# Kernel tuning notes

Measured on AMD Instinct MI355X. Metric: run time of the kernel, lower is better.

The kernel has to match this reference:

```python
import jax, jax.numpy as jnp
import numpy as np

N = 100000      # total nodes (10 graphs x 10000)
E = 1600000     # edges, avg degree 16
HN = 64         # hidden_node_dim
HE = 16         # hidden_edge_dim
IN_N, IN_E = 3, 1
L = 3           # conv_layers
B = 10          # num_graphs
NEG_SLOPE = 0.2
BN_EPS = 1e-5


def setup_inputs() -> dict:
    key = jax.random.key(0)
    ks = jax.random.split(key, 8)
    s = lambda d: 1.0 / np.sqrt(d)
    return {
        "x": jax.random.normal(ks[0], (N, IN_N), jnp.float32),
        "edge_attr": jax.random.uniform(ks[1], (E, IN_E), jnp.float32),
        "edge_index": jax.random.randint(ks[2], (2, E), 0, N, jnp.int64),
        "fc_node_w": jax.random.normal(ks[3], (IN_N, HN), jnp.float32) * s(IN_N),
        "fc_node_b": jnp.zeros((HN,), jnp.float32),
        "fc_edge_w": jax.random.normal(ks[4], (IN_E, HE), jnp.float32) * s(IN_E),
        "fc_edge_b": jnp.zeros((HE,), jnp.float32),
        "bn_gamma": jnp.ones((HN,), jnp.float32),
        "bn_beta": jnp.zeros((HN,), jnp.float32),
        "fc_w": jax.random.normal(ks[5], (L, HN, HN), jnp.float32) * s(HN),
        "fc_b": jnp.zeros((L, HN), jnp.float32),
        "attn_w": jax.random.normal(ks[6], (L, 2 * HN + HE, HN), jnp.float32) * s(2 * HN + HE),
        "attn_b": jnp.zeros((L, HN), jnp.float32),
        "batch_size": B,
    }


def segment_softmax(alpha, idx, num_segments):
    # PyG softmax: per-target-node, per-channel, numerically stable
    amax = jax.ops.segment_max(alpha, idx, num_segments=num_segments)
    amax = jnp.where(jnp.isfinite(amax), amax, 0.0)  # empty segments -> -inf
    ex = jnp.exp(alpha - amax[idx])
    denom = jax.ops.segment_sum(ex, idx, num_segments=num_segments)
    return ex / (denom[idx] + 1e-16)


def reference(x, edge_attr, edge_index, fc_node_w, fc_node_b, fc_edge_w, fc_edge_b,
              bn_gamma, bn_beta, fc_w, fc_b, attn_w, attn_b, batch_size):
    h = x @ fc_node_w + fc_node_b                 # [N, HN]
    e = edge_attr @ fc_edge_w + fc_edge_b        # [E, HE]
    # BatchNorm1d (training-mode batch statistics, biased variance)
    mean = jnp.mean(h, axis=0)
    var = jnp.mean((h - mean) ** 2, axis=0)
    h = (h - mean) * jax.lax.rsqrt(var + BN_EPS) * bn_gamma + bn_beta

    src, dst = edge_index[0], edge_index[1]      # x_j = h[src], x_i = h[dst]
    for l in range(L):
        hl = h @ fc_w[l] + fc_b[l]               # [N, HN]
        xi = hl[dst]                             # [E, HN]
        xj = hl[src]                             # [E, HN]
        cat = jnp.concatenate([xi, xj, e], axis=-1)  # [E, 2*HN+HE]
        alpha = cat @ attn_w[l] + attn_b[l]      # [E, HN]
        alpha = jax.nn.leaky_relu(alpha, NEG_SLOPE)
        alpha = segment_softmax(alpha, dst, N)
        h = jax.ops.segment_sum(xj * alpha, dst, num_segments=N)  # scatter-add aggregate
    return h.reshape(batch_size, -1, HN)
```

## Files before the change

kernel.cpp:

```cpp
#include <hip/hip_runtime.h>
#include <math.h>

#define NN 100000
#define NE 1600000
#define LAYERS 3
#define NEG 0.2f
#define BN_EPS 1e-5f
#define LOG2E 1.4426950408889634f

#define NB 196
#define NWG 512
#define CHUNK 3125
#define MOMB 304
#define TFB 1563

typedef __attribute__((ext_vector_type(8))) short bf16x8;
typedef __attribute__((ext_vector_type(4))) float f32x4;

#if __has_builtin(__builtin_amdgcn_exp2f)
#define EXP2(x) __builtin_amdgcn_exp2f(x)
#else
#define EXP2(x) __expf((x) * 0.6931471805599453f)
#endif

__device__ __forceinline__ unsigned f2bf(float x) {
    unsigned u = __float_as_uint(x);
    return (u + 0x7fffu + ((u >> 16) & 1u)) >> 16;
}

__global__ __launch_bounds__(256) void k_front(const int* __restrict__ ei,
    int* __restrict__ counts, const float* __restrict__ x, float* __restrict__ mom)
{
    int t = threadIdx.x;
    if (blockIdx.x < NWG) {
        __shared__ int hist[NB];
        int wg = blockIdx.x;
        if (t < NB) hist[t] = 0;
        __syncthreads();
        int base = wg * CHUNK;
        for (int i = t; i < CHUNK; i += 256)
            atomicAdd(&hist[ei[NE + base + i] >> 9], 1);
        __syncthreads();
        if (t < NB) counts[wg * NB + t] = hist[t];
    } else {
        int mb = blockIdx.x - NWG;
        float s0=0,s1=0,s2=0,m00=0,m01=0,m02=0,m11=0,m12=0,m22=0;
        for (int n = mb * 256 + t; n < NN; n += MOMB * 256) {
            float a = x[n*3], b = x[n*3+1], c = x[n*3+2];
            s0 += a; s1 += b; s2 += c;
            m00 = fmaf(a,a,m00); m01 = fmaf(a,b,m01); m02 = fmaf(a,c,m02);
            m11 = fmaf(b,b,m11); m12 = fmaf(b,c,m12); m22 = fmaf(c,c,m22);
        }
        #pragma unroll
        for (int off = 32; off; off >>= 1) {
            s0 += __shfl_xor(s0, off); s1 += __shfl_xor(s1, off); s2 += __shfl_xor(s2, off);
            m00 += __shfl_xor(m00, off); m01 += __shfl_xor(m01, off); m02 += __shfl_xor(m02, off);
            m11 += __shfl_xor(m11, off); m12 += __shfl_xor(m12, off); m22 += __shfl_xor(m22, off);
        }
        __shared__ float red[4][9];
        int wave = t >> 6, lane = t & 63;
        if (lane == 0) {
            red[wave][0]=s0; red[wave][1]=s1; red[wave][2]=s2;
            red[wave][3]=m00; red[wave][4]=m01; red[wave][5]=m02;
            red[wave][6]=m11; red[wave][7]=m12; red[wave][8]=m22;
        }
        __syncthreads();
        if (t < 9) {
            float v = red[0][t] + red[1][t] + red[2][t] + red[3][t];
            atomicAdd(&mom[t], v);
        }
    }
}

__device__ __forceinline__ float bn_scale_of(const float* __restrict__ mom,
    const float* __restrict__ fnw, const float* __restrict__ fnb,
    const float* __restrict__ gamma, int k)
{
    float w0 = fnw[k], w1 = fnw[64 + k], w2 = fnw[128 + k], bc = fnb[k];
    float dot  = mom[0]*w0 + mom[1]*w1 + mom[2]*w2;
    float quad = mom[3]*w0*w0 + 2.f*mom[4]*w0*w1 + 2.f*mom[5]*w0*w2
               + mom[6]*w1*w1 + 2.f*mom[7]*w1*w2 + mom[8]*w2*w2;
    float mean = dot * (1.0f / NN) + bc;
    float eh2  = quad * (1.0f / NN) + 2.f * bc * dot * (1.0f / NN) + bc * bc;
    float var  = eh2 - mean * mean;
    return gamma[k] * rsqrtf(var + BN_EPS);
}

__global__ __launch_bounds__(256) void k_mid(const float* __restrict__ mom,
    const float* __restrict__ fnw, const float* __restrict__ fnb,
    const float* __restrict__ gamma, const float* __restrict__ beta,
    const float* __restrict__ few, const float* __restrict__ feb,
    const float* __restrict__ attn_w, const float* __restrict__ attn_b,
    const float* __restrict__ fcb, const float* __restrict__ fcw,
    int* __restrict__ counts, int* __restrict__ bbase, int* __restrict__ row_ptr,
    float* __restrict__ u, float* __restrict__ c0, float* __restrict__ feff,
    unsigned short* __restrict__ wt)
{
    int t = threadIdx.x;
    if (blockIdx.x == 0) {
        __shared__ float ssh[64], sfe[3][64];
        if (t < 64) {
            float w0 = fnw[t], w1 = fnw[64 + t], w2 = fnw[128 + t], bc = fnb[t];
            float dot  = mom[0]*w0 + mom[1]*w1 + mom[2]*w2;
            float quad = mom[3]*w0*w0 + 2.f*mom[4]*w0*w1 + 2.f*mom[5]*w0*w2
                       + mom[6]*w1*w1 + 2.f*mom[7]*w1*w2 + mom[8]*w2*w2;
            float mean = dot * (1.0f / NN) + bc;
            float eh2  = quad * (1.0f / NN) + 2.f * bc * dot * (1.0f / NN) + bc * bc;
            float var  = eh2 - mean * mean;
            float sc   = gamma[t] * rsqrtf(var + BN_EPS);
            ssh[t] = beta[t] - mean * sc;
        }
        __syncthreads();
        if (t < 64) {
            float v = 0.f;
            for (int k = 0; k < 64; k++) v = fmaf(ssh[k], fcw[k * 64 + t], v);
            sfe[0][t] = fcb[t] + v;
            sfe[1][t] = fcb[64 + t];
            sfe[2][t] = fcb[128 + t];
        }
        __syncthreads();
        if (t < 192) {
            int l = t >> 6, c = t & 63;
            const float* AW = attn_w + l * 144 * 64;
            float uu = 0.f, cc = 0.f;
            for (int j = 0; j < 16; j++) {
                float wv = AW[(128 + j) * 64 + c];
                uu = fmaf(few[j], wv, uu);
                cc = fmaf(feb[j], wv, cc);
            }
            float bi = 0.f;
            for (int tt = 0; tt < 64; tt++)
                bi = fmaf(sfe[l][tt], AW[tt * 64 + c] + AW[(64 + tt) * 64 + c], bi);
            u[t]    = uu * LOG2E;
            c0[t]   = (cc + attn_b[t] + bi) * LOG2E;
            feff[t] = sfe[l][c];
        }
    } else if (blockIdx.x == 1) {
        __shared__ int s_tot[256];
        int tot = 0;
        if (t < NB)
            for (int w = 0; w < NWG; w++) tot += counts[w * NB + t];
        s_tot[t] = tot;
        __syncthreads();
        for (int off = 1; off < 256; off <<= 1) {
            int v = (t >= off) ? s_tot[t - off] : 0;
            __syncthreads();
            s_tot[t] += v;
            __syncthreads();
        }
        int excl = s_tot[t] - tot;
        if (t < NB) {
            bbase[t] = excl;
            int run = excl;
            for (int w = 0; w < NWG; w++) {
                int c = counts[w * NB + t];
                counts[w * NB + t] = run;
                run += c;
            }
            if (t == NB - 1) {
                bbase[NB] = run;
                row_ptr[NN] = run;
            }
        }
    } else {
        int task = (blockIdx.x - 2) * 4 + (t >> 6);
        int k = t & 63;
        int l = task / 192, g = task - l * 192;
        const float* W0 = fcw + l * 4096;
        float scale = (l == 0) ? bn_scale_of(mom, fnw, fnb, gamma, k) : 1.0f;
        float v;
        if (g < 64) {
            v = W0[k * 64 + g] * scale;
        } else {
            int c = g & 63;
            const float* Wx = attn_w + l * 144 * 64 + (g < 128 ? 0 : 4096);
            float s = 0.f;
            for (int tt = 0; tt < 64; tt++) s = fmaf(W0[k * 64 + tt], Wx[tt * 64 + c], s);
            v = s * scale * LOG2E;
        }
        wt[(l * 192 + g) * 64 + k] = (unsigned short)f2bf(v);
    }
}

__device__ __forceinline__ void tf_core(const bf16x8* a, const unsigned short* __restrict__ wt_l,
    const float* __restrict__ feff_l, const float* __restrict__ c0_l,
    float* __restrict__ ai, unsigned* __restrict__ packed, int n0, int r16, int quad)
{
    f32x4 acc[12];
    #pragma unroll
    for (int i = 0; i < 12; i++) acc[i] = (f32x4){0.f, 0.f, 0.f, 0.f};
    const unsigned short* wb = wt_l + (size_t)r16 * 64 + quad * 8;
    #pragma unroll
    for (int cb = 0; cb < 12; cb++) {
        bf16x8 b0 = *(const bf16x8*)(wb + cb * 1024);
        bf16x8 b1 = *(const bf16x8*)(wb + cb * 1024 + 32);
        acc[cb] = __builtin_amdgcn_mfma_f32_16x16x32_bf16(a[0], b0, acc[cb], 0, 0, 0);
        acc[cb] = __builtin_amdgcn_mfma_f32_16x16x32_bf16(a[1], b1, acc[cb], 0, 0, 0);
    }
    #pragma unroll
    for (int r = 0; r < 4; r++) {
        int nd = n0 + quad * 4 + r;
        if (nd < NN) {
            size_t base = (size_t)nd * 64 + r16;
            #pragma unroll
            for (int cq = 0; cq < 4; cq++) {
                float hlv = acc[cq][r] + feff_l[cq * 16 + r16];
                float aiv = acc[4 + cq][r] + c0_l[cq * 16 + r16];
                float ajv = acc[8 + cq][r];
                ai[base + cq * 16]     = aiv;
                packed[base + cq * 16] = f2bf(hlv) | (f2bf(ajv) << 16);
            }
        }
    }
}

__global__ __launch_bounds__(256) void k_l3(const int* __restrict__ ei,
    const float* __restrict__ ea, const int* __restrict__ counts, int2* __restrict__ brec,
    const float* __restrict__ xin, const float* __restrict__ fnw, const float* __restrict__ fnb,
    const unsigned short* __restrict__ wt, const float* __restrict__ feff,
    const float* __restrict__ c0v, float* __restrict__ ai, unsigned* __restrict__ packed)
{
    int t = threadIdx.x;
    if (blockIdx.x < NWG) {
        __shared__ int off[NB];
        int wg = blockIdx.x;
        if (t < NB) off[t] = counts[wg * NB + t];
        __syncthreads();
        int base = wg * CHUNK;
        for (int i = t; i < CHUNK; i += 256) {
            int k = base + i;
            int s = ei[k], d = ei[NE + k];
            int b = d >> 9;
            int j = atomicAdd(&off[b], 1);
            brec[j] = make_int2(((d & 511) << 17) | s, __float_as_int(ea[k]));
        }
    } else {
        int bid = blockIdx.x - NWG;
        int wv = t >> 6, l = t & 63;
        int r16 = l & 15, quad = l >> 4;
        int n0 = bid * 64 + wv * 16;
        int na = n0 + r16; if (na >= NN) na = NN - 1;
        float x0 = xin[na*3], x1 = xin[na*3+1], x2 = xin[na*3+2];
        bf16x8 a[2];
        #pragma unroll
        for (int ks = 0; ks < 2; ks++) {
            bf16x8 tt;
            #pragma unroll
            for (int e = 0; e < 8; e++) {
                int c = quad * 8 + ks * 32 + e;
                float v = fmaf(x0, fnw[c], fmaf(x1, fnw[64 + c], fmaf(x2, fnw[128 + c], fnb[c])));
                tt[e] = (short)f2bf(v);
            }
            a[ks] = tt;
        }
        tf_core(a, wt, feff, c0v, ai, packed, n0, r16, quad);
    }
}

__global__ __launch_bounds__(256) void k_csr(const int2* __restrict__ brec,
    const int* __restrict__ bbase, int* __restrict__ row_ptr, int2* __restrict__ er)
{
    __shared__ int s_cnt[512], s_excl[512], s_ts[256];
    int t = threadIdx.x, b = blockIdx.x;
    int beg = bbase[b], end = bbase[b + 1];
    s_cnt[t] = 0; s_cnt[t + 256] = 0;
    __syncthreads();
    for (int i = beg + t; i < end; i += 256)
        atomicAdd(&s_cnt[brec[i].x >> 17], 1);
    __syncthreads();
    int a0 = s_cnt[2 * t], a1 = s_cnt[2 * t + 1];
    int ts = a0 + a1;
    s_ts[t] = ts;
    __syncthreads();
    for (int off = 1; off < 256; off <<= 1) {
        int v = (t >= off) ? s_ts[t - off] : 0;
        __syncthreads();
        s_ts[t] += v;
        __syncthreads();
    }
    int et = s_ts[t] - ts;
    s_excl[2 * t] = et; s_excl[2 * t + 1] = et + a0;
    s_cnt[t] = 0; s_cnt[t + 256] = 0;
    __syncthreads();
    #pragma unroll
    for (int q = 0; q < 2; q++) {
        int dl = t + q * 256;
        int n = b * 512 + dl;
        if (n < NN) row_ptr[n] = beg + s_excl[dl];
    }
    for (int i = beg + t; i < end; i += 256) {
        int2 r = brec[i];
        int dl = r.x >> 17;
        int pos = atomicAdd(&s_cnt[dl], 1);
        er[beg + s_excl[dl] + pos] = make_int2(r.x & 0x1FFFF, r.y);
    }
}

#define EDGE_STEP(q, dacc, sacc) { \
    float aa = fmaf(__int_as_float(e[q].y), uc, base + __uint_as_float(p[q] & 0xffff0000u)); \
    aa = fmaxf(aa, NEG * aa); \
    float xx = EXP2(aa); \
    dacc += xx; sacc = fmaf(xx, __uint_as_float(p[q] << 16), sacc); }

template<int DOTF>
__global__ __launch_bounds__(256) void k_edgetf(const unsigned* __restrict__ packed_r,
    float* __restrict__ ai, const int* __restrict__ row_ptr,
    const int2* __restrict__ er, const float* __restrict__ u_l,
    const unsigned short* __restrict__ wt_n, const float* __restrict__ feff_n,
    const float* __restrict__ c0_n, unsigned* __restrict__ packed_w,
    float* __restrict__ outp)
{
    __shared__ float hlds[64][68];
    int t = threadIdx.x;
    int wv = t >> 6, lane = t & 63;
    int nbase = blockIdx.x * 64 + wv * 16;
    float uc = u_l[lane];
    const unsigned* __restrict__ pc = packed_r + lane;
    for (int m = 0; m < 16; m++) {
        int n = nbase + m;
        if (n >= NN) break;
        int beg = row_ptr[n], end = row_ptr[n + 1];
        float base = ai[(size_t)n * 64 + lane];
        float d0 = 0.f, d1 = 0.f, s0 = 0.f, s1 = 0.f;
        int k = beg;
        for (; k + 16 <= end; k += 16) {
            int2 e[16]; unsigned p[16];
            #pragma unroll
            for (int q = 0; q < 16; q++) e[q] = er[k + q];
            #pragma unroll
            for (int q = 0; q < 16; q++) p[q] = pc[(size_t)e[q].x << 6];
            #pragma unroll
            for (int q = 0; q < 16; q++) {
                if (q & 1) EDGE_STEP(q, d1, s1) else EDGE_STEP(q, d0, s0)
            }
        }
        for (; k + 8 <= end; k += 8) {
            int2 e[8]; unsigned p[8];
            #pragma unroll
            for (int q = 0; q < 8; q++) e[q] = er[k + q];
            #pragma unroll
            for (int q = 0; q < 8; q++) p[q] = pc[(size_t)e[q].x << 6];
            #pragma unroll
            for (int q = 0; q < 8; q++) {
                if (q & 1) EDGE_STEP(q, d1, s1) else EDGE_STEP(q, d0, s0)
            }
        }
        for (; k + 4 <= end; k += 4) {
            int2 e[4]; unsigned p[4];
            #pragma unroll
            for (int q = 0; q < 4; q++) e[q] = er[k + q];
            #pragma unroll
            for (int q = 0; q < 4; q++) p[q] = pc[(size_t)e[q].x << 6];
            #pragma unroll
            for (int q = 0; q < 4; q++) {
                if (q & 1) EDGE_STEP(q, d1, s1) else EDGE_STEP(q, d0, s0)
            }
        }
        for (; k < end; k++) {
            int2 e[1]; unsigned p[1];
            e[0] = er[k];
            p[0] = pc[(size_t)e[0].x << 6];
            EDGE_STEP(0, d0, s0)
        }
        float hv = (s0 + s1) / (d0 + d1 + 1e-16f);
        if (DOTF) hlds[wv * 16 + m][lane] = hv;
        else      outp[(size_t)n * 64 + lane] = hv;
    }
    if (DOTF) {
        int r16 = lane & 15, quad = lane >> 4;
        const float* hp = &hlds[wv * 16 + r16][quad * 8];
        bf16x8 a[2];
        #pragma unroll
        for (int ks = 0; ks < 2; ks++) {
            f32x4 lo = *(const f32x4*)(hp + ks * 32);
            f32x4 hi = *(const f32x4*)(hp + ks * 32 + 4);
            bf16x8 tt;
            tt[0] = (short)f2bf(lo[0]); tt[1] = (short)f2bf(lo[1]);
            tt[2] = (short)f2bf(lo[2]); tt[3] = (short)f2bf(lo[3]);
            tt[4] = (short)f2bf(hi[0]); tt[5] = (short)f2bf(hi[1]);
            tt[6] = (short)f2bf(hi[2]); tt[7] = (short)f2bf(hi[3]);
            a[ks] = tt;
        }
        tf_core(a, wt_n, feff_n, c0_n, ai, packed_w, nbase, r16, quad);
    }
}

extern "C" void kernel_launch(void* const* d_in, const int* in_sizes, int n_in,
                              void* d_out, int out_size, void* d_ws, size_t ws_size,
                              hipStream_t stream)
{
    const float* x    = (const float*)d_in[0];
    const float* ea   = (const float*)d_in[1];
    const int*   ei   = (const int*)d_in[2];
    const float* fnw  = (const float*)d_in[3];
    const float* fnb  = (const float*)d_in[4];
    const float* few  = (const float*)d_in[5];
    const float* feb  = (const float*)d_in[6];
    const float* gmm  = (const float*)d_in[7];
    const float* beta = (const float*)d_in[8];
    const float* fcw  = (const float*)d_in[9];
    const float* fcb  = (const float*)d_in[10];
    const float* aw   = (const float*)d_in[11];
    const float* ab   = (const float*)d_in[12];
    float* out = (float*)d_out;

    char* ws = (char*)d_ws;
    size_t off = 0;
    auto alloc = [&](size_t bytes) -> void* {
        void* p = ws + off;
        off += (bytes + 255) / 256 * 256;
        return p;
    };
    float*    ai      = (float*)   alloc((size_t)NN * 64 * 4);
    unsigned* packed0 = (unsigned*)alloc((size_t)NN * 64 * 4);
    unsigned* packed1 = (unsigned*)alloc((size_t)NN * 64 * 4);
    int2*     er      = (int2*)    alloc((size_t)NE * 8);
    int2*     brec    = (int2*)    alloc((size_t)NE * 8);
    int*      row_ptr = (int*)     alloc((size_t)(NN + 1) * 4);
    int*      counts  = (int*)     alloc((size_t)NB * NWG * 4);
    int*      bbase   = (int*)     alloc((NB + 1) * 4);
    float*    mom     = (float*)   alloc(12 * 4);
    float*    uvec    = (float*)   alloc(192 * 4);
    float*    c0vec   = (float*)   alloc(192 * 4);
    float*    feff    = (float*)   alloc(192 * 4);
    unsigned short* wt = (unsigned short*)alloc((size_t)LAYERS * 192 * 64 * 2);

    (void)hipMemsetAsync(mom, 0, 12 * 4, stream);

    k_front<<<NWG + MOMB, 256, 0, stream>>>(ei, counts, x, mom);
    k_mid<<<2 + 144, 256, 0, stream>>>(mom, fnw, fnb, gmm, beta, few, feb, aw, ab,
                                       fcb, fcw, counts, bbase, row_ptr,
                                       uvec, c0vec, feff, wt);
    k_l3<<<NWG + TFB, 256, 0, stream>>>(ei, ea, counts, brec, x, fnw, fnb,
                                        wt, feff, c0vec, ai, packed0);
    k_csr<<<NB, 256, 0, stream>>>(brec, bbase, row_ptr, er);
    k_edgetf<1><<<TFB, 256, 0, stream>>>(packed0, ai, row_ptr, er, uvec,
                                         wt + (size_t)192 * 64, feff + 64, c0vec + 64,
                                         packed1, out);
    k_edgetf<1><<<TFB, 256, 0, stream>>>(packed1, ai, row_ptr, er, uvec + 64,
                                         wt + (size_t)2 * 192 * 64, feff + 128, c0vec + 128,
                                         packed0, out);
    k_edgetf<0><<<TFB, 256, 0, stream>>>(packed0, ai, row_ptr, er, uvec + 128,
                                         wt, feff, c0vec, packed1, out);
    (void)in_sizes; (void)n_in; (void)out_size; (void)ws_size;
}
```

Measured before the change: 497.1 us.

## Assign one node per wave in edge-aggregation kernel with 1024-thread blocks

The edge softmax-aggregation kernel now gives each wave a single destination node instead of looping over 16 nodes per wave. Blocks grow to 16 waves (1024 threads), and 16 times as many waves are in flight across the GPU. After a block barrier, four of the waves each compute one 16-column slice of the next layer's transform with MFMA. The transform helper is also reorganised to hold fewer accumulators at once, which lowers register pressure. The aim is to hide gather latency and balance uneven node degrees, at the cost of a block-wide sync and 12 idle waves during the MFMA step.

```diff
diff --git a/kernel.cpp b/kernel.cpp
--- a/kernel.cpp
+++ b/kernel.cpp
@@ -13,6 +13,7 @@
 #define CHUNK 3125
 #define MOMB 304
 #define TFB 1563
+#define ETB 6250
 
 typedef __attribute__((ext_vector_type(8))) short bf16x8;
 typedef __attribute__((ext_vector_type(4))) float f32x4;
@@ -186,29 +187,24 @@
     const float* __restrict__ feff_l, const float* __restrict__ c0_l,
     float* __restrict__ ai, unsigned* __restrict__ packed, int n0, int r16, int quad)
 {
-    f32x4 acc[12];
-    #pragma unroll
-    for (int i = 0; i < 12; i++) acc[i] = (f32x4){0.f, 0.f, 0.f, 0.f};
     const unsigned short* wb = wt_l + (size_t)r16 * 64 + quad * 8;
     #pragma unroll
-    for (int cb = 0; cb < 12; cb++) {
-        bf16x8 b0 = *(const bf16x8*)(wb + cb * 1024);
-        bf16x8 b1 = *(const bf16x8*)(wb + cb * 1024 + 32);
-        acc[cb] = __builtin_amdgcn_mfma_f32_16x16x32_bf16(a[0], b0, acc[cb], 0, 0, 0);
-        acc[cb] = __builtin_amdgcn_mfma_f32_16x16x32_bf16(a[1], b1, acc[cb], 0, 0, 0);
-    }
-    #pragma unroll
-    for (int r = 0; r < 4; r++) {
-        int nd = n0 + quad * 4 + r;
-        if (nd < NN) {
-            size_t base = (size_t)nd * 64 + r16;
-            #pragma unroll
-            for (int cq = 0; cq < 4; cq++) {
-                float hlv = acc[cq][r] + feff_l[cq * 16 + r16];
-                float aiv = acc[4 + cq][r] + c0_l[cq * 16 + r16];
-                float ajv = acc[8 + cq][r];
-                ai[base + cq * 16]     = aiv;
-                packed[base + cq * 16] = f2bf(hlv) | (f2bf(ajv) << 16);
+    for (int cq = 0; cq < 4; cq++) {
+        f32x4 ah = {0.f,0.f,0.f,0.f}, aa = {0.f,0.f,0.f,0.f}, aj = {0.f,0.f,0.f,0.f};
+        ah = __builtin_amdgcn_mfma_f32_16x16x32_bf16(a[0], *(const bf16x8*)(wb + cq * 1024), ah, 0, 0, 0);
+        ah = __builtin_amdgcn_mfma_f32_16x16x32_bf16(a[1], *(const bf16x8*)(wb + cq * 1024 + 32), ah, 0, 0, 0);
+        aa = __builtin_amdgcn_mfma_f32_16x16x32_bf16(a[0], *(const bf16x8*)(wb + (4 + cq) * 1024), aa, 0, 0, 0);
+        aa = __builtin_amdgcn_mfma_f32_16x16x32_bf16(a[1], *(const bf16x8*)(wb + (4 + cq) * 1024 + 32), aa, 0, 0, 0);
+        aj = __builtin_amdgcn_mfma_f32_16x16x32_bf16(a[0], *(const bf16x8*)(wb + (8 + cq) * 1024), aj, 0, 0, 0);
+        aj = __builtin_amdgcn_mfma_f32_16x16x32_bf16(a[1], *(const bf16x8*)(wb + (8 + cq) * 1024 + 32), aj, 0, 0, 0);
+        float fe = feff_l[cq * 16 + r16], cc = c0_l[cq * 16 + r16];
+        #pragma unroll
+        for (int r = 0; r < 4; r++) {
+            int nd = n0 + quad * 4 + r;
+            if (nd < NN) {
+                size_t base = (size_t)nd * 64 + cq * 16 + r16;
+                ai[base]     = aa[r] + cc;
+                packed[base] = f2bf(ah[r] + fe) | (f2bf(aj[r]) << 16);
             }
         }
     }
@@ -303,85 +299,101 @@
     dacc += xx; sacc = fmaf(xx, __uint_as_float(p[q] << 16), sacc); }
 
 template<int DOTF>
-__global__ __launch_bounds__(256) void k_edgetf(const unsigned* __restrict__ packed_r,
+__global__ __launch_bounds__(1024) void k_edgetf(const unsigned* __restrict__ packed_r,
     float* __restrict__ ai, const int* __restrict__ row_ptr,
     const int2* __restrict__ er, const float* __restrict__ u_l,
     const unsigned short* __restrict__ wt_n, const float* __restrict__ feff_n,
     const float* __restrict__ c0_n, unsigned* __restrict__ packed_w,
     float* __restrict__ outp)
 {
-    __shared__ float hlds[64][68];
+    __shared__ float hlds[16][68];
     int t = threadIdx.x;
     int wv = t >> 6, lane = t & 63;
-    int nbase = blockIdx.x * 64 + wv * 16;
+    int n = blockIdx.x * 16 + wv;
+    int beg = row_ptr[n], end = row_ptr[n + 1];
+    float base = ai[(size_t)n * 64 + lane];
     float uc = u_l[lane];
     const unsigned* __restrict__ pc = packed_r + lane;
-    for (int m = 0; m < 16; m++) {
-        int n = nbase + m;
-        if (n >= NN) break;
-        int beg = row_ptr[n], end = row_ptr[n + 1];
-        float base = ai[(size_t)n * 64 + lane];
-        float d0 = 0.f, d1 = 0.f, s0 = 0.f, s1 = 0.f;
-        int k = beg;
-        for (; k + 16 <= end; k += 16) {
-            int2 e[16]; unsigned p[16];
+    float d0 = 0.f, d1 = 0.f, s0 = 0.f, s1 = 0.f;
+    int k = beg;
+    for (; k + 16 <= end; k += 16) {
+        int2 e[16]; unsigned p[16];
+        #pragma unroll
+        for (int q = 0; q < 16; q++) e[q] = er[k + q];
+        #pragma unroll
+        for (int q = 0; q < 16; q++) p[q] = pc[(size_t)e[q].x << 6];
+        #pragma unroll
+        for (int q = 0; q < 16; q++) {
+            if (q & 1) EDGE_STEP(q, d1, s1) else EDGE_STEP(q, d0, s0)
+        }
+    }
+    for (; k + 8 <= end; k += 8) {
+        int2 e[8]; unsigned p[8];
+        #pragma unroll
+        for (int q = 0; q < 8; q++) e[q] = er[k + q];
+        #pragma unroll
+        for (int q = 0; q < 8; q++) p[q] = pc[(size_t)e[q].x << 6];
+        #pragma unroll
+        for (int q = 0; q < 8; q++) {
+            if (q & 1) EDGE_STEP(q, d1, s1) else EDGE_STEP(q, d0, s0)
+        }
+    }
+    for (; k + 4 <= end; k += 4) {
+        int2 e[4]; unsigned p[4];
+        #pragma unroll
+        for (int q = 0; q < 4; q++) e[q] = er[k + q];
+        #pragma unroll
+        for (int q = 0; q < 4; q++) p[q] = pc[(size_t)e[q].x << 6];
+        #pragma unroll
+        for (int q = 0; q < 4; q++) {
+            if (q & 1) EDGE_STEP(q, d1, s1) else EDGE_STEP(q, d0, s0)
+        }
+    }
+    for (; k < end; k++) {
+        int2 e[1]; unsigned p[1];
+        e[0] = er[k];
+        p[0] = pc[(size_t)e[0].x << 6];
+        EDGE_STEP(0, d0, s0)
+    }
+    float hv = (s0 + s1) / (d0 + d1 + 1e-16f);
+    if (DOTF) {
+        hlds[wv][lane] = hv;
+        __syncthreads();
+        if (wv < 4) {
+            int r16 = lane & 15, quad = lane >> 4;
+            const float* hp = &hlds[r16][quad * 8];
+            bf16x8 a[2];
             #pragma unroll
-            for (int q = 0; q < 16; q++) e[q] = er[k + q];
+            for (int ks = 0; ks < 2; ks++) {
+                f32x4 lo = *(const f32x4*)(hp + ks * 32);
+                f32x4 hi = *(const f32x4*)(hp + ks * 32 + 4);
+                bf16x8 tt;
+                tt[0] = (short)f2bf(lo[0]); tt[1] = (short)f2bf(lo[1]);
+                tt[2] = (short)f2bf(lo[2]); tt[3] = (short)f2bf(lo[3]);
+                tt[4] = (short)f2bf(hi[0]); tt[5] = (short)f2bf(hi[1]);
+                tt[6] = (short)f2bf(hi[2]); tt[7] = (short)f2bf(hi[3]);
+                a[ks] = tt;
+            }
+            const unsigned short* wb = wt_n + (size_t)r16 * 64 + quad * 8;
+            int cq = wv;
+            f32x4 ah = {0.f,0.f,0.f,0.f}, aa = {0.f,0.f,0.f,0.f}, aj = {0.f,0.f,0.f,0.f};
+            ah = __builtin_amdgcn_mfma_f32_16x16x32_bf16(a[0], *(const bf16x8*)(wb + cq * 1024), ah, 0, 0, 0);
+            ah = __builtin_amdgcn_mfma_f32_16x16x32_bf16(a[1], *(const bf16x8*)(wb + cq * 1024 + 32), ah, 0, 0, 0);
+            aa = __builtin_amdgcn_mfma_f32_16x16x32_bf16(a[0], *(const bf16x8*)(wb + (4 + cq) * 1024), aa, 0, 0, 0);
+            aa = __builtin_amdgcn_mfma_f32_16x16x32_bf16(a[1], *(const bf16x8*)(wb + (4 + cq) * 1024 + 32), aa, 0, 0, 0);
+            aj = __builtin_amdgcn_mfma_f32_16x16x32_bf16(a[0], *(const bf16x8*)(wb + (8 + cq) * 1024), aj, 0, 0, 0);
+            aj = __builtin_amdgcn_mfma_f32_16x16x32_bf16(a[1], *(const bf16x8*)(wb + (8 + cq) * 1024 + 32), aj, 0, 0, 0);
+            float fe = feff_n[cq * 16 + r16], cc = c0_n[cq * 16 + r16];
             #pragma unroll
-            for (int q = 0; q < 16; q++) p[q] = pc[(size_t)e[q].x << 6];
-            #pragma unroll
-            for (int q = 0; q < 16; q++) {
-                if (q & 1) EDGE_STEP(q, d1, s1) else EDGE_STEP(q, d0, s0)
-            }
-        }
-        for (; k + 8 <= end; k += 8) {
-            int2 e[8]; unsigned p[8];
-            #pragma unroll
-            for (int q = 0; q < 8; q++) e[q] = er[k + q];
-            #pragma unroll
-            for (int q = 0; q < 8; q++) p[q] = pc[(size_t)e[q].x << 6];
-            #pragma unroll
-            for (int q = 0; q < 8; q++) {
-                if (q & 1) EDGE_STEP(q, d1, s1) else EDGE_STEP(q, d0, s0)
-            }
-        }
-        for (; k + 4 <= end; k += 4) {
-            int2 e[4]; unsigned p[4];
-            #pragma unroll
-            for (int q = 0; q < 4; q++) e[q] = er[k + q];
-            #pragma unroll
-            for (int q = 0; q < 4; q++) p[q] = pc[(size_t)e[q].x << 6];
-            #pragma unroll
-            for (int q = 0; q < 4; q++) {
-                if (q & 1) EDGE_STEP(q, d1, s1) else EDGE_STEP(q, d0, s0)
-            }
-        }
-        for (; k < end; k++) {
-            int2 e[1]; unsigned p[1];
-            e[0] = er[k];
-            p[0] = pc[(size_t)e[0].x << 6];
-            EDGE_STEP(0, d0, s0)
-        }
-        float hv = (s0 + s1) / (d0 + d1 + 1e-16f);
-        if (DOTF) hlds[wv * 16 + m][lane] = hv;
-        else      outp[(size_t)n * 64 + lane] = hv;
-    }
-    if (DOTF) {
-        int r16 = lane & 15, quad = lane >> 4;
-        const float* hp = &hlds[wv * 16 + r16][quad * 8];
-        bf16x8 a[2];
-        #pragma unroll
-        for (int ks = 0; ks < 2; ks++) {
-            f32x4 lo = *(const f32x4*)(hp + ks * 32);
-            f32x4 hi = *(const f32x4*)(hp + ks * 32 + 4);
-            bf16x8 tt;
-            tt[0] = (short)f2bf(lo[0]); tt[1] = (short)f2bf(lo[1]);
-            tt[2] = (short)f2bf(lo[2]); tt[3] = (short)f2bf(lo[3]);
-            tt[4] = (short)f2bf(hi[0]); tt[5] = (short)f2bf(hi[1]);
-            tt[6] = (short)f2bf(hi[2]); tt[7] = (short)f2bf(hi[3]);
-            a[ks] = tt;
-        }
-        tf_core(a, wt_n, feff_n, c0_n, ai, packed_w, nbase, r16, quad);
+            for (int r = 0; r < 4; r++) {
+                int nd = blockIdx.x * 16 + quad * 4 + r;
+                size_t ob = (size_t)nd * 64 + cq * 16 + r16;
+                ai[ob]       = aa[r] + cc;
+                packed_w[ob] = f2bf(ah[r] + fe) | (f2bf(aj[r]) << 16);
+            }
+        }
+    } else {
+        outp[(size_t)n * 64 + lane] = hv;
     }
 }
 
@@ -434,13 +446,13 @@
     k_l3<<<NWG + TFB, 256, 0, stream>>>(ei, ea, counts, brec, x, fnw, fnb,
                                         wt, feff, c0vec, ai, packed0);
     k_csr<<<NB, 256, 0, stream>>>(brec, bbase, row_ptr, er);
-    k_edgetf<1><<<TFB, 256, 0, stream>>>(packed0, ai, row_ptr, er, uvec,
-                                         wt + (size_t)192 * 64, feff + 64, c0vec + 64,
-                                         packed1, out);
-    k_edgetf<1><<<TFB, 256, 0, stream>>>(packed1, ai, row_ptr, er, uvec + 64,
-                                         wt + (size_t)2 * 192 * 64, feff + 128, c0vec + 128,
-                                         packed0, out);
-    k_edgetf<0><<<TFB, 256, 0, stream>>>(packed0, ai, row_ptr, er, uvec + 128,
-                                         wt, feff, c0vec, packed1, out);
+    k_edgetf<1><<<ETB, 1024, 0, stream>>>(packed0, ai, row_ptr, er, uvec,
+                                          wt + (size_t)192 * 64, feff + 64, c0vec + 64,
+                                          packed1, out);
+    k_edgetf<1><<<ETB, 1024, 0, stream>>>(packed1, ai, row_ptr, er, uvec + 64,
+                                          wt + (size_t)2 * 192 * 64, feff + 128, c0vec + 128,
+                                          packed0, out);
+    k_edgetf<0><<<ETB, 1024, 0, stream>>>(packed0, ai, row_ptr, er, uvec + 128,
+                                          wt, feff, c0vec, packed1, out);
     (void)in_sizes; (void)n_in; (void)out_size; (void)ws_size;
 }
```

Result: slower. 510.7 us (+2.7%).
